# Kernel optimization log

Measured on AMD Instinct MI355X. Metric: run time of the kernel, lower is better.

## Reference

```python
import jax, jax.numpy as jnp
import numpy as np
import math

N = 50000          # n_nodes
E = 1600000        # n_edges (avg degree 32)
D = 256            # input_size
H = 8              # n_heads
HS = D // H        # head_size = 32


def setup_inputs() -> dict:
    key = jax.random.key(0)
    k1, k2, k3, k4, k5 = jax.random.split(key, 5)
    X = jax.random.normal(k1, (N, D), dtype=jnp.float32)
    # xavier_uniform for [D, HS] weight: bound = sqrt(6 / (fan_in + fan_out))
    bound = math.sqrt(6.0 / (D + HS))
    Wq = jax.random.uniform(k2, (D, HS), jnp.float32, -bound, bound)
    Wk = jax.random.uniform(k3, (D, HS), jnp.float32, -bound, bound)
    Wv = jax.random.uniform(k4, (D, HS), jnp.float32, -bound, bound)
    edge_index = jax.random.randint(k5, (2, E), 0, N, dtype=jnp.int32)
    return {"X": X, "Wq": Wq, "Wk": Wk, "Wv": Wv, "edge_index": edge_index}


def reference(X, Wq, Wk, Wv, edge_index):
    # Projections: [N, HS]
    Q = X @ Wq
    K = X @ Wk
    V = X @ Wv
    r = edge_index[0]  # row (query) node per edge
    c = edge_index[1]  # col (key/value) node per edge
    dk = jnp.asarray(math.sqrt(HS), dtype=X.dtype)
    # Edge-level attention logits: [E]
    scores = jnp.sum(Q[r] * K[c], axis=-1) / dk
    # Sparse row-wise (dim=1) softmax over existing edges only.
    row_max = jax.ops.segment_max(scores, r, num_segments=N)   # -inf for empty rows
    ex = jnp.exp(scores - row_max[r])                          # [E]
    denom = jax.ops.segment_sum(ex, r, num_segments=N)         # [N]
    # Weighted V aggregation: [N, HS]
    num = jax.ops.segment_sum(ex[:, None] * V[c], r, num_segments=N)
    # Rows with no incident edges produce zeros (matches sparse softmax + to_dense @ V).
    safe = jnp.maximum(denom, jnp.asarray(1e-30, X.dtype))[:, None]
    return jnp.where(denom[:, None] > 0, num / safe, jnp.zeros_like(num))
```

## Files before the change

kernel.cpp:

```cpp
#include <hip/hip_runtime.h>

#define N_NODES 50000
#define N_EDGES 1600000
#define D_IN    256
#define HS      32

#define NB      400
#define ROWS_PB 125
#define CAP     5120
#define EPB     4096

#define MTILE   64
#define PROJ_B  ((N_NODES + MTILE - 1) / MTILE)
#define BIN_B   ((N_EDGES + EPB - 1) / EPB)

typedef __bf16 bf16x8 __attribute__((ext_vector_type(8)));
typedef float  floatx4 __attribute__((ext_vector_type(4)));

static __device__ __forceinline__ unsigned short f2bf(float f) {
    unsigned u = __float_as_uint(f);
    return (unsigned short)((u + 0x7FFFu + ((u >> 16) & 1u)) >> 16);
}

__global__ __launch_bounds__(256) void wfrag_kernel(
    const float* __restrict__ Wq, const float* __restrict__ Wk,
    const float* __restrict__ Wv, unsigned short* __restrict__ wfrag,
    int* __restrict__ fill, int* __restrict__ rowptr)
{
    if (blockIdx.x == 0) {
        for (int b = threadIdx.x; b < NB; b += 256) fill[b] = 0;
        if (threadIdx.x == 0) rowptr[N_NODES] = N_EDGES;
    }
    const int i = blockIdx.x * blockDim.x + threadIdx.x;
    if (i >= 8 * 6 * 64 * 8) return;
    const int j    = i & 7;
    const int lane = (i >> 3) & 63;
    const int st   = i >> 9;
    const int t    = st % 6;
    const int s    = st / 6;
    const int k    = s * 32 + (lane >> 4) * 8 + j;
    const int col  = t * 16 + (lane & 15);
    float v;
    if      (col < 32) v = Wq[k * HS + col];
    else if (col < 64) v = Wk[k * HS + (col - 32)];
    else               v = Wv[k * HS + (col - 64)];
    wfrag[i] = f2bf(v);
}

__global__ __launch_bounds__(256) void proj_bin_kernel(
    const float* __restrict__ X, const unsigned short* __restrict__ wfrag,
    float* __restrict__ Q, unsigned int* __restrict__ KVp,
    const int* __restrict__ er, const int* __restrict__ ec,
    int* __restrict__ fill, unsigned int* __restrict__ pairs)
{
    __shared__ int lcnt[NB];

    const int t = threadIdx.x;
    const int mod = blockIdx.x % 3;

    if (mod != 2) {
        const int pb   = (blockIdx.x / 3) * 2 + mod;
        const int lane = t & 63;
        const int w    = t >> 6;
        const int quad = lane >> 4;
        const int m16  = lane & 15;
        const int row0 = pb * MTILE;

        int ar = row0 + w * 16 + m16;
        if (ar >= N_NODES) ar = N_NODES - 1;
        const float* xrow = X + (size_t)ar * D_IN;

        floatx4 acc[6];
#pragma unroll
        for (int nt = 0; nt < 6; nt++) acc[nt] = (floatx4)0.f;

#pragma unroll
        for (int s = 0; s < 8; s++) {
            const float4 xa = *(const float4*)(xrow + s * 32 + quad * 8);
            const float4 xb = *(const float4*)(xrow + s * 32 + quad * 8 + 4);
            bf16x8 bfr[6];
#pragma unroll
            for (int nt = 0; nt < 6; nt++)
                bfr[nt] = *(const bf16x8*)(wfrag + (((s * 6 + nt) * 64 + lane) * 8));
            union { bf16x8 v; unsigned short u[8]; } afr;
            afr.u[0] = f2bf(xa.x); afr.u[1] = f2bf(xa.y);
            afr.u[2] = f2bf(xa.z); afr.u[3] = f2bf(xa.w);
            afr.u[4] = f2bf(xb.x); afr.u[5] = f2bf(xb.y);
            afr.u[6] = f2bf(xb.z); afr.u[7] = f2bf(xb.w);
#pragma unroll
            for (int nt = 0; nt < 6; nt++)
                acc[nt] = __builtin_amdgcn_mfma_f32_16x16x32_bf16(afr.v, bfr[nt], acc[nt], 0, 0, 0);
        }

#pragma unroll
        for (int i = 0; i < 4; i++) {
            const int gr = row0 + w * 16 + quad * 4 + i;
            if (gr < N_NODES) {
#pragma unroll
                for (int nt = 0; nt < 2; nt++)
                    Q[gr * HS + nt * 16 + m16] = acc[nt][i];
#pragma unroll
                for (int p = 0; p < 2; p++) {
                    const int j = p * 16 + m16;
                    const unsigned kb = f2bf(acc[2 + p][i]);
                    const unsigned vb = f2bf(acc[4 + p][i]);
                    KVp[gr * HS + j] = (kb << 16) | vb;
                }
            }
        }
    } else {
        const int bb = blockIdx.x / 3;
        const int e0 = bb * EPB;
        const int e1 = min(e0 + EPB, N_EDGES);

        for (int b = t; b < NB; b += 256) lcnt[b] = 0;
        __syncthreads();

        int rl[16], cl[16];
#pragma unroll
        for (int i = 0; i < 16; i++) {
            const int e = e0 + t + i * 256;
            if (e < e1) {
                rl[i] = er[e];
                cl[i] = ec[e];
                atomicAdd(&lcnt[rl[i] / ROWS_PB], 1);
            }
        }
        __syncthreads();

        for (int b = t; b < NB; b += 256) {
            const int c = lcnt[b];
            lcnt[b] = (c > 0) ? atomicAdd(&fill[b], c) : 0;
        }
        __syncthreads();

#pragma unroll
        for (int i = 0; i < 16; i++) {
            const int e = e0 + t + i * 256;
            if (e < e1) {
                const int r = rl[i];
                const int b = r / ROWS_PB;
                const int slot = atomicAdd(&lcnt[b], 1);
                pairs[(size_t)b * CAP + slot] =
                    ((unsigned)(r - b * ROWS_PB) << 16) | (unsigned)cl[i];
            }
        }
    }
}

__global__ __launch_bounds__(256) void place_kernel(
    const unsigned int* __restrict__ pairs, const int* __restrict__ fill,
    int* __restrict__ rowptr, int* __restrict__ col_sorted)
{
    __shared__ int cnt_l[ROWS_PB];
    __shared__ int s[128];
    __shared__ int red[256];
    __shared__ int stage[CAP];

    const int b = blockIdx.x;
    const int t = threadIdx.x;
    const int n = fill[b];
    const unsigned int* pb = pairs + (size_t)b * CAP;

    int partial = 0;
    for (int i = t; i < b; i += 256) partial += fill[i];
    red[t] = partial;
    for (int i = t; i < ROWS_PB; i += 256) cnt_l[i] = 0;
    __syncthreads();
#pragma unroll
    for (int ofs = 128; ofs > 0; ofs >>= 1) {
        if (t < ofs) red[t] += red[t + ofs];
        __syncthreads();
    }
    const int base = red[0];

    unsigned pl[20];
#pragma unroll
    for (int k = 0; k < 20; k++) {
        const int i = t + k * 256;
        if (i < n) {
            pl[k] = pb[i];
            atomicAdd(&cnt_l[pl[k] >> 16], 1);
        }
    }
    __syncthreads();

    if (t < 128) s[t] = (t < ROWS_PB) ? cnt_l[t] : 0;
    __syncthreads();
#pragma unroll
    for (int ofs = 1; ofs < 128; ofs <<= 1) {
        const int u = (t < 128 && t >= ofs) ? s[t - ofs] : 0;
        __syncthreads();
        if (t < 128) s[t] += u;
        __syncthreads();
    }
    int excl = 0;
    if (t < ROWS_PB) {
        excl = s[t] - cnt_l[t];
        rowptr[b * ROWS_PB + t] = base + excl;
    }
    __syncthreads();
    if (t < ROWS_PB) cnt_l[t] = excl;
    __syncthreads();

#pragma unroll
    for (int k = 0; k < 20; k++) {
        const int i = t + k * 256;
        if (i < n) {
            const unsigned p = pl[k];
            const int pos = atomicAdd(&cnt_l[p >> 16], 1);
            stage[pos] = (int)(p & 0xFFFFu);
        }
    }
    __syncthreads();

    for (int i = t; i < n; i += 256)
        col_sorted[base + i] = stage[i];
}

__global__ __launch_bounds__(256) void aggregate_kernel(
    const int* __restrict__ rowptr, const int* __restrict__ col,
    const float* __restrict__ Q, const unsigned int* __restrict__ KVp,
    float* __restrict__ out)
{
    const int lane = threadIdx.x & 63;
    const int r    = (blockIdx.x * blockDim.x + threadIdx.x) >> 6;
    if (r >= N_NODES) return;
    const int comp = lane & 7;
    const int slot = lane >> 3;

    const float4 q4 = *(const float4*)(Q + r * HS + comp * 4);
    const int start = rowptr[r];
    const int end   = rowptr[r + 1];
    const int last  = end - 1;
    const float scale = 0.17677669529663687f;

    float accD = 0.f;
    float n0 = 0.f, n1 = 0.f, n2 = 0.f, n3 = 0.f;

    for (int e0 = start; e0 < end; e0 += 32) {
        int   cc[4];
        uint4 kv[4];
#pragma unroll
        for (int b = 0; b < 4; b++)
            if (e0 + 8 * b < end)
                cc[b] = col[min(e0 + 8 * b + slot, last)];
#pragma unroll
        for (int b = 0; b < 4; b++)
            if (e0 + 8 * b < end)
                kv[b] = *(const uint4*)(KVp + (size_t)cc[b] * HS + comp * 4);
#pragma unroll
        for (int b = 0; b < 4; b++) {
            if (e0 + 8 * b < end) {
                float p = q4.x * __uint_as_float(kv[b].x & 0xFFFF0000u)
                        + q4.y * __uint_as_float(kv[b].y & 0xFFFF0000u)
                        + q4.z * __uint_as_float(kv[b].z & 0xFFFF0000u)
                        + q4.w * __uint_as_float(kv[b].w & 0xFFFF0000u);
#pragma unroll
                for (int ofs = 1; ofs < 8; ofs <<= 1)
                    p += __shfl_xor(p, ofs, 64);
                const float ex = (e0 + 8 * b + slot < end) ? __expf(p * scale) : 0.f;
                accD += ex;
                n0 += ex * __uint_as_float(kv[b].x << 16);
                n1 += ex * __uint_as_float(kv[b].y << 16);
                n2 += ex * __uint_as_float(kv[b].z << 16);
                n3 += ex * __uint_as_float(kv[b].w << 16);
            }
        }
    }

#pragma unroll
    for (int ofs = 8; ofs < 64; ofs <<= 1) {
        accD += __shfl_xor(accD, ofs, 64);
        n0 += __shfl_xor(n0, ofs, 64);
        n1 += __shfl_xor(n1, ofs, 64);
        n2 += __shfl_xor(n2, ofs, 64);
        n3 += __shfl_xor(n3, ofs, 64);
    }

    if (slot == 0) {
        const float inv = (accD > 0.f) ? 1.f / accD : 0.f;
        float4 o;
        o.x = n0 * inv; o.y = n1 * inv; o.z = n2 * inv; o.w = n3 * inv;
        *(float4*)(out + r * HS + comp * 4) = o;
    }
}

extern "C" void kernel_launch(void* const* d_in, const int* in_sizes, int n_in,
                              void* d_out, int out_size, void* d_ws, size_t ws_size,
                              hipStream_t stream)
{
    const float* X  = (const float*)d_in[0];
    const float* Wq = (const float*)d_in[1];
    const float* Wk = (const float*)d_in[2];
    const float* Wv = (const float*)d_in[3];
    const int*   ei = (const int*)d_in[4];
    const int* er = ei;
    const int* ec = ei + N_EDGES;

    float* out = (float*)d_out;

    float* Q          = (float*)d_ws;
    unsigned int* KVp = (unsigned int*)(Q + (size_t)N_NODES * HS);
    int* fill         = (int*)(KVp + (size_t)N_NODES * HS);
    int* rowptr       = fill + NB;
    unsigned short* wfrag = (unsigned short*)(rowptr + (N_NODES + 1));
    unsigned int* pairs   = (unsigned int*)(wfrag + 8 * 6 * 64 * 8);
    int* col_sorted   = (int*)(pairs + (size_t)NB * CAP);

    wfrag_kernel<<<(8 * 6 * 64 * 8 + 255) / 256, 256, 0, stream>>>(
        Wq, Wk, Wv, wfrag, fill, rowptr);

    proj_bin_kernel<<<PROJ_B + BIN_B, 256, 0, stream>>>(
        X, wfrag, Q, KVp, er, ec, fill, pairs);

    place_kernel<<<NB, 256, 0, stream>>>(pairs, fill, rowptr, col_sorted);

    aggregate_kernel<<<(N_NODES * 64 + 255) / 256, 256, 0, stream>>>(
        rowptr, col_sorted, Q, KVp, out);
}
```

Baseline: 159.7 us.

## Regroup stages: bin with weight packing, then place with projection

Reorganizes the launch schedule. Edge binning now shares one launch with weight-fragment packing, and bucket placement shares one launch with the MFMA projection. The fill counter reset moves to a memset. Placement also writes straight to global col_sorted instead of staging through a 20KB LDS buffer. The aim is to overlap independent work and cut a launch, at the cost of scattered global writes in the place stage.

```diff
diff --git a/kernel.cpp b/kernel.cpp
--- a/kernel.cpp
+++ b/kernel.cpp
@@ -13,6 +13,7 @@
 #define MTILE   64
 #define PROJ_B  ((N_NODES + MTILE - 1) / MTILE)
 #define BIN_B   ((N_EDGES + EPB - 1) / EPB)
+#define WFRAG_B 6
 
 typedef __bf16 bf16x8 __attribute__((ext_vector_type(8)));
 typedef float  floatx4 __attribute__((ext_vector_type(4)));
@@ -22,95 +23,17 @@
     return (unsigned short)((u + 0x7FFFu + ((u >> 16) & 1u)) >> 16);
 }
 
-__global__ __launch_bounds__(256) void wfrag_kernel(
+__global__ __launch_bounds__(256) void bin_wfrag_kernel(
+    const int* __restrict__ er, const int* __restrict__ ec,
+    int* __restrict__ fill, unsigned int* __restrict__ pairs,
     const float* __restrict__ Wq, const float* __restrict__ Wk,
-    const float* __restrict__ Wv, unsigned short* __restrict__ wfrag,
-    int* __restrict__ fill, int* __restrict__ rowptr)
-{
-    if (blockIdx.x == 0) {
-        for (int b = threadIdx.x; b < NB; b += 256) fill[b] = 0;
-        if (threadIdx.x == 0) rowptr[N_NODES] = N_EDGES;
-    }
-    const int i = blockIdx.x * blockDim.x + threadIdx.x;
-    if (i >= 8 * 6 * 64 * 8) return;
-    const int j    = i & 7;
-    const int lane = (i >> 3) & 63;
-    const int st   = i >> 9;
-    const int t    = st % 6;
-    const int s    = st / 6;
-    const int k    = s * 32 + (lane >> 4) * 8 + j;
-    const int col  = t * 16 + (lane & 15);
-    float v;
-    if      (col < 32) v = Wq[k * HS + col];
-    else if (col < 64) v = Wk[k * HS + (col - 32)];
-    else               v = Wv[k * HS + (col - 64)];
-    wfrag[i] = f2bf(v);
-}
-
-__global__ __launch_bounds__(256) void proj_bin_kernel(
-    const float* __restrict__ X, const unsigned short* __restrict__ wfrag,
-    float* __restrict__ Q, unsigned int* __restrict__ KVp,
-    const int* __restrict__ er, const int* __restrict__ ec,
-    int* __restrict__ fill, unsigned int* __restrict__ pairs)
+    const float* __restrict__ Wv, unsigned short* __restrict__ wfrag)
 {
     __shared__ int lcnt[NB];
-
     const int t = threadIdx.x;
-    const int mod = blockIdx.x % 3;
-
-    if (mod != 2) {
-        const int pb   = (blockIdx.x / 3) * 2 + mod;
-        const int lane = t & 63;
-        const int w    = t >> 6;
-        const int quad = lane >> 4;
-        const int m16  = lane & 15;
-        const int row0 = pb * MTILE;
-
-        int ar = row0 + w * 16 + m16;
-        if (ar >= N_NODES) ar = N_NODES - 1;
-        const float* xrow = X + (size_t)ar * D_IN;
-
-        floatx4 acc[6];
-#pragma unroll
-        for (int nt = 0; nt < 6; nt++) acc[nt] = (floatx4)0.f;
-
-#pragma unroll
-        for (int s = 0; s < 8; s++) {
-            const float4 xa = *(const float4*)(xrow + s * 32 + quad * 8);
-            const float4 xb = *(const float4*)(xrow + s * 32 + quad * 8 + 4);
-            bf16x8 bfr[6];
-#pragma unroll
-            for (int nt = 0; nt < 6; nt++)
-                bfr[nt] = *(const bf16x8*)(wfrag + (((s * 6 + nt) * 64 + lane) * 8));
-            union { bf16x8 v; unsigned short u[8]; } afr;
-            afr.u[0] = f2bf(xa.x); afr.u[1] = f2bf(xa.y);
-            afr.u[2] = f2bf(xa.z); afr.u[3] = f2bf(xa.w);
-            afr.u[4] = f2bf(xb.x); afr.u[5] = f2bf(xb.y);
-            afr.u[6] = f2bf(xb.z); afr.u[7] = f2bf(xb.w);
-#pragma unroll
-            for (int nt = 0; nt < 6; nt++)
-                acc[nt] = __builtin_amdgcn_mfma_f32_16x16x32_bf16(afr.v, bfr[nt], acc[nt], 0, 0, 0);
-        }
-
-#pragma unroll
-        for (int i = 0; i < 4; i++) {
-            const int gr = row0 + w * 16 + quad * 4 + i;
-            if (gr < N_NODES) {
-#pragma unroll
-                for (int nt = 0; nt < 2; nt++)
-                    Q[gr * HS + nt * 16 + m16] = acc[nt][i];
-#pragma unroll
-                for (int p = 0; p < 2; p++) {
-                    const int j = p * 16 + m16;
-                    const unsigned kb = f2bf(acc[2 + p][i]);
-                    const unsigned vb = f2bf(acc[4 + p][i]);
-                    KVp[gr * HS + j] = (kb << 16) | vb;
-                }
-            }
-        }
-    } else {
-        const int bb = blockIdx.x / 3;
-        const int e0 = bb * EPB;
+
+    if (blockIdx.x < BIN_B) {
+        const int e0 = blockIdx.x * EPB;
         const int e1 = min(e0 + EPB, N_EDGES);
 
         for (int b = t; b < NB; b += 256) lcnt[b] = 0;
@@ -145,77 +68,146 @@
                     ((unsigned)(r - b * ROWS_PB) << 16) | (unsigned)cl[i];
             }
         }
-    }
-}
-
-__global__ __launch_bounds__(256) void place_kernel(
+    } else {
+        const int wb = blockIdx.x - BIN_B;
+#pragma unroll
+        for (int ii = 0; ii < 16; ii++) {
+            const int i = wb * 4096 + ii * 256 + t;
+            const int j    = i & 7;
+            const int lane = (i >> 3) & 63;
+            const int st   = i >> 9;
+            const int tt   = st % 6;
+            const int s    = st / 6;
+            const int k    = s * 32 + (lane >> 4) * 8 + j;
+            const int col  = tt * 16 + (lane & 15);
+            float v;
+            if      (col < 32) v = Wq[k * HS + col];
+            else if (col < 64) v = Wk[k * HS + (col - 32)];
+            else               v = Wv[k * HS + (col - 64)];
+            wfrag[i] = f2bf(v);
+        }
+    }
+}
+
+__global__ __launch_bounds__(256) void place_proj_kernel(
     const unsigned int* __restrict__ pairs, const int* __restrict__ fill,
-    int* __restrict__ rowptr, int* __restrict__ col_sorted)
+    int* __restrict__ rowptr, int* __restrict__ col_sorted,
+    const float* __restrict__ X, const unsigned short* __restrict__ wfrag,
+    float* __restrict__ Q, unsigned int* __restrict__ KVp)
 {
     __shared__ int cnt_l[ROWS_PB];
     __shared__ int s[128];
     __shared__ int red[256];
-    __shared__ int stage[CAP];
-
-    const int b = blockIdx.x;
+
     const int t = threadIdx.x;
-    const int n = fill[b];
-    const unsigned int* pb = pairs + (size_t)b * CAP;
-
-    int partial = 0;
-    for (int i = t; i < b; i += 256) partial += fill[i];
-    red[t] = partial;
-    for (int i = t; i < ROWS_PB; i += 256) cnt_l[i] = 0;
-    __syncthreads();
-#pragma unroll
-    for (int ofs = 128; ofs > 0; ofs >>= 1) {
-        if (t < ofs) red[t] += red[t + ofs];
-        __syncthreads();
-    }
-    const int base = red[0];
-
-    unsigned pl[20];
-#pragma unroll
-    for (int k = 0; k < 20; k++) {
-        const int i = t + k * 256;
-        if (i < n) {
-            pl[k] = pb[i];
-            atomicAdd(&cnt_l[pl[k] >> 16], 1);
-        }
-    }
-    __syncthreads();
-
-    if (t < 128) s[t] = (t < ROWS_PB) ? cnt_l[t] : 0;
-    __syncthreads();
-#pragma unroll
-    for (int ofs = 1; ofs < 128; ofs <<= 1) {
-        const int u = (t < 128 && t >= ofs) ? s[t - ofs] : 0;
-        __syncthreads();
-        if (t < 128) s[t] += u;
-        __syncthreads();
-    }
-    int excl = 0;
-    if (t < ROWS_PB) {
-        excl = s[t] - cnt_l[t];
-        rowptr[b * ROWS_PB + t] = base + excl;
-    }
-    __syncthreads();
-    if (t < ROWS_PB) cnt_l[t] = excl;
-    __syncthreads();
-
-#pragma unroll
-    for (int k = 0; k < 20; k++) {
-        const int i = t + k * 256;
-        if (i < n) {
-            const unsigned p = pl[k];
-            const int pos = atomicAdd(&cnt_l[p >> 16], 1);
-            stage[pos] = (int)(p & 0xFFFFu);
-        }
-    }
-    __syncthreads();
-
-    for (int i = t; i < n; i += 256)
-        col_sorted[base + i] = stage[i];
+
+    if (blockIdx.x < NB) {
+        const int b = blockIdx.x;
+        const int n = fill[b];
+        const unsigned int* pb = pairs + (size_t)b * CAP;
+
+        int partial = 0;
+        for (int i = t; i < b; i += 256) partial += fill[i];
+        red[t] = partial;
+        for (int i = t; i < ROWS_PB; i += 256) cnt_l[i] = 0;
+        __syncthreads();
+#pragma unroll
+        for (int ofs = 128; ofs > 0; ofs >>= 1) {
+            if (t < ofs) red[t] += red[t + ofs];
+            __syncthreads();
+        }
+        const int base = red[0];
+
+        unsigned pl[20];
+#pragma unroll
+        for (int k = 0; k < 20; k++) {
+            const int i = t + k * 256;
+            if (i < n) {
+                pl[k] = pb[i];
+                atomicAdd(&cnt_l[pl[k] >> 16], 1);
+            }
+        }
+        __syncthreads();
+
+        if (t < 128) s[t] = (t < ROWS_PB) ? cnt_l[t] : 0;
+        __syncthreads();
+#pragma unroll
+        for (int ofs = 1; ofs < 128; ofs <<= 1) {
+            const int u = (t < 128 && t >= ofs) ? s[t - ofs] : 0;
+            __syncthreads();
+            if (t < 128) s[t] += u;
+            __syncthreads();
+        }
+        int gcur = 0;
+        if (t < ROWS_PB) {
+            gcur = base + s[t] - cnt_l[t];
+            rowptr[b * ROWS_PB + t] = gcur;
+        }
+        __syncthreads();
+        if (t < ROWS_PB) cnt_l[t] = gcur;
+        if (b == NB - 1 && t == 0) rowptr[N_NODES] = N_EDGES;
+        __syncthreads();
+
+#pragma unroll
+        for (int k = 0; k < 20; k++) {
+            const int i = t + k * 256;
+            if (i < n) {
+                const unsigned p = pl[k];
+                const int pos = atomicAdd(&cnt_l[p >> 16], 1);
+                col_sorted[pos] = (int)(p & 0xFFFFu);
+            }
+        }
+    } else {
+        const int pb   = blockIdx.x - NB;
+        const int lane = t & 63;
+        const int w    = t >> 6;
+        const int quad = lane >> 4;
+        const int m16  = lane & 15;
+        const int row0 = pb * MTILE;
+
+        int ar = row0 + w * 16 + m16;
+        if (ar >= N_NODES) ar = N_NODES - 1;
+        const float* xrow = X + (size_t)ar * D_IN;
+
+        floatx4 acc[6];
+#pragma unroll
+        for (int nt = 0; nt < 6; nt++) acc[nt] = (floatx4)0.f;
+
+#pragma unroll
+        for (int ss = 0; ss < 8; ss++) {
+            const float4 xa = *(const float4*)(xrow + ss * 32 + quad * 8);
+            const float4 xb = *(const float4*)(xrow + ss * 32 + quad * 8 + 4);
+            bf16x8 bfr[6];
+#pragma unroll
+            for (int nt = 0; nt < 6; nt++)
+                bfr[nt] = *(const bf16x8*)(wfrag + (((ss * 6 + nt) * 64 + lane) * 8));
+            union { bf16x8 v; unsigned short u[8]; } afr;
+            afr.u[0] = f2bf(xa.x); afr.u[1] = f2bf(xa.y);
+            afr.u[2] = f2bf(xa.z); afr.u[3] = f2bf(xa.w);
+            afr.u[4] = f2bf(xb.x); afr.u[5] = f2bf(xb.y);
+            afr.u[6] = f2bf(xb.z); afr.u[7] = f2bf(xb.w);
+#pragma unroll
+            for (int nt = 0; nt < 6; nt++)
+                acc[nt] = __builtin_amdgcn_mfma_f32_16x16x32_bf16(afr.v, bfr[nt], acc[nt], 0, 0, 0);
+        }
+
+#pragma unroll
+        for (int i = 0; i < 4; i++) {
+            const int gr = row0 + w * 16 + quad * 4 + i;
+            if (gr < N_NODES) {
+#pragma unroll
+                for (int nt = 0; nt < 2; nt++)
+                    Q[gr * HS + nt * 16 + m16] = acc[nt][i];
+#pragma unroll
+                for (int p = 0; p < 2; p++) {
+                    const int j = p * 16 + m16;
+                    const unsigned kb = f2bf(acc[2 + p][i]);
+                    const unsigned vb = f2bf(acc[4 + p][i]);
+                    KVp[gr * HS + j] = (kb << 16) | vb;
+                }
+            }
+        }
+    }
 }
 
 __global__ __launch_bounds__(256) void aggregate_kernel(
@@ -308,13 +300,13 @@
     unsigned int* pairs   = (unsigned int*)(wfrag + 8 * 6 * 64 * 8);
     int* col_sorted   = (int*)(pairs + (size_t)NB * CAP);
 
-    wfrag_kernel<<<(8 * 6 * 64 * 8 + 255) / 256, 256, 0, stream>>>(
-        Wq, Wk, Wv, wfrag, fill, rowptr);
-
-    proj_bin_kernel<<<PROJ_B + BIN_B, 256, 0, stream>>>(
-        X, wfrag, Q, KVp, er, ec, fill, pairs);
-
-    place_kernel<<<NB, 256, 0, stream>>>(pairs, fill, rowptr, col_sorted);
+    hipMemsetAsync(fill, 0, NB * sizeof(int), stream);
+
+    bin_wfrag_kernel<<<BIN_B + WFRAG_B, 256, 0, stream>>>(
+        er, ec, fill, pairs, Wq, Wk, Wv, wfrag);
+
+    place_proj_kernel<<<NB + PROJ_B, 256, 0, stream>>>(
+        pairs, fill, rowptr, col_sorted, X, wfrag, Q, KVp);
 
     aggregate_kernel<<<(N_NODES * 64 + 255) / 256, 256, 0, stream>>>(
         rowptr, col_sorted, Q, KVp, out);
```

New measurement: 162.4 us. No clear change (+1.7%).

## Schedule larger edge-binning blocks first in fused projection/binning kernel

Applied to the files above, without the earlier changes.

Raises edges per binning block from 4096 to 16384, so there are fewer binning blocks and fewer global atomics on the fill counters. Binning blocks now take the first block indices instead of being interleaved with projection blocks, so the long-running binning work is dispatched first. The edges are streamed with a loop that re-reads the row index in the second pass instead of keeping them in registers. A launch-bounds occupancy hint is added. The risk is that the few heavy binning blocks dominate the tail, and the second pass adds extra global reads.

```diff
diff --git a/kernel.cpp b/kernel.cpp
--- a/kernel.cpp
+++ b/kernel.cpp
@@ -8,11 +8,12 @@
 #define NB      400
 #define ROWS_PB 125
 #define CAP     5120
-#define EPB     4096
+
+#define EPB     16384
+#define BIN_B   ((N_EDGES + EPB - 1) / EPB)
 
 #define MTILE   64
 #define PROJ_B  ((N_NODES + MTILE - 1) / MTILE)
-#define BIN_B   ((N_EDGES + EPB - 1) / EPB)
 
 typedef __bf16 bf16x8 __attribute__((ext_vector_type(8)));
 typedef float  floatx4 __attribute__((ext_vector_type(4)));
@@ -47,19 +48,41 @@
     wfrag[i] = f2bf(v);
 }
 
-__global__ __launch_bounds__(256) void proj_bin_kernel(
+__global__ __launch_bounds__(256, 6) void proj_bin_kernel(
     const float* __restrict__ X, const unsigned short* __restrict__ wfrag,
     float* __restrict__ Q, unsigned int* __restrict__ KVp,
     const int* __restrict__ er, const int* __restrict__ ec,
     int* __restrict__ fill, unsigned int* __restrict__ pairs)
 {
     __shared__ int lcnt[NB];
-
     const int t = threadIdx.x;
-    const int mod = blockIdx.x % 3;
-
-    if (mod != 2) {
-        const int pb   = (blockIdx.x / 3) * 2 + mod;
+
+    if (blockIdx.x < BIN_B) {
+        const int e0 = blockIdx.x * EPB;
+        const int e1 = min(e0 + EPB, N_EDGES);
+
+        for (int b = t; b < NB; b += 256) lcnt[b] = 0;
+        __syncthreads();
+
+        for (int e = e0 + t; e < e1; e += 256)
+            atomicAdd(&lcnt[er[e] / ROWS_PB], 1);
+        __syncthreads();
+
+        for (int b = t; b < NB; b += 256) {
+            const int c = lcnt[b];
+            lcnt[b] = (c > 0) ? atomicAdd(&fill[b], c) : 0;
+        }
+        __syncthreads();
+
+        for (int e = e0 + t; e < e1; e += 256) {
+            const int r = er[e];
+            const int b = r / ROWS_PB;
+            const int slot = atomicAdd(&lcnt[b], 1);
+            pairs[(size_t)b * CAP + slot] =
+                ((unsigned)(r - b * ROWS_PB) << 16) | (unsigned)ec[e];
+        }
+    } else {
+        const int pb   = blockIdx.x - BIN_B;
         const int lane = t & 63;
         const int w    = t >> 6;
         const int quad = lane >> 4;
@@ -75,13 +98,13 @@
         for (int nt = 0; nt < 6; nt++) acc[nt] = (floatx4)0.f;
 
 #pragma unroll
-        for (int s = 0; s < 8; s++) {
-            const float4 xa = *(const float4*)(xrow + s * 32 + quad * 8);
-            const float4 xb = *(const float4*)(xrow + s * 32 + quad * 8 + 4);
+        for (int ss = 0; ss < 8; ss++) {
+            const float4 xa = *(const float4*)(xrow + ss * 32 + quad * 8);
+            const float4 xb = *(const float4*)(xrow + ss * 32 + quad * 8 + 4);
             bf16x8 bfr[6];
 #pragma unroll
             for (int nt = 0; nt < 6; nt++)
-                bfr[nt] = *(const bf16x8*)(wfrag + (((s * 6 + nt) * 64 + lane) * 8));
+                bfr[nt] = *(const bf16x8*)(wfrag + (((ss * 6 + nt) * 64 + lane) * 8));
             union { bf16x8 v; unsigned short u[8]; } afr;
             afr.u[0] = f2bf(xa.x); afr.u[1] = f2bf(xa.y);
             afr.u[2] = f2bf(xa.z); afr.u[3] = f2bf(xa.w);
@@ -106,43 +129,6 @@
                     const unsigned vb = f2bf(acc[4 + p][i]);
                     KVp[gr * HS + j] = (kb << 16) | vb;
                 }
-            }
-        }
-    } else {
-        const int bb = blockIdx.x / 3;
-        const int e0 = bb * EPB;
-        const int e1 = min(e0 + EPB, N_EDGES);
-
-        for (int b = t; b < NB; b += 256) lcnt[b] = 0;
-        __syncthreads();
-
-        int rl[16], cl[16];
-#pragma unroll
-        for (int i = 0; i < 16; i++) {
-            const int e = e0 + t + i * 256;
-            if (e < e1) {
-                rl[i] = er[e];
-                cl[i] = ec[e];
-                atomicAdd(&lcnt[rl[i] / ROWS_PB], 1);
-            }
-        }
-        __syncthreads();
-
-        for (int b = t; b < NB; b += 256) {
-            const int c = lcnt[b];
-            lcnt[b] = (c > 0) ? atomicAdd(&fill[b], c) : 0;
-        }
-        __syncthreads();
-
-#pragma unroll
-        for (int i = 0; i < 16; i++) {
-            const int e = e0 + t + i * 256;
-            if (e < e1) {
-                const int r = rl[i];
-                const int b = r / ROWS_PB;
-                const int slot = atomicAdd(&lcnt[b], 1);
-                pairs[(size_t)b * CAP + slot] =
-                    ((unsigned)(r - b * ROWS_PB) << 16) | (unsigned)cl[i];
             }
         }
     }
@@ -311,7 +297,7 @@
     wfrag_kernel<<<(8 * 6 * 64 * 8 + 255) / 256, 256, 0, stream>>>(
         Wq, Wk, Wv, wfrag, fill, rowptr);
 
-    proj_bin_kernel<<<PROJ_B + BIN_B, 256, 0, stream>>>(
+    proj_bin_kernel<<<BIN_B + PROJ_B, 256, 0, stream>>>(
         X, wfrag, Q, KVp, er, ec, fill, pairs);
 
     place_kernel<<<NB, 256, 0, stream>>>(pairs, fill, rowptr, col_sorted);
```

Measured after the change: 189.3 us. 18.5% more time.
